# Optimization experiments

Measured on AMD Instinct MI355X. Metric: run time of the kernel, lower is better.

Reference implementation:

```python
import jax, jax.numpy as jnp
import numpy as np

B, N_LR, N_HR, D, NH, L, K = 16, 256, 512, 512, 8, 4, 4
FF = 4 * D

def _ln(x, g, b):
    m = jnp.mean(x, -1, keepdims=True)
    v = jnp.var(x, -1, keepdims=True)
    return (x - m) * jax.lax.rsqrt(v + 1e-5) * g + b

def _gelu(x):
    return jax.nn.gelu(x, approximate=False)  # torch nn.GELU default = exact

def _attn(x, qkvW, qkvb, projW, projb, bias):
    b, n, d = x.shape
    hd = d // NH
    qkv = (x @ qkvW + qkvb).reshape(b, n, 3, NH, hd).transpose(2, 0, 3, 1, 4)
    q, k, v = qkv[0], qkv[1], qkv[2]
    a = jnp.einsum('bhnd,bhmd->bhnm', q, k) * (hd ** -0.5)
    if bias is not None:
        a = a + bias
    a = jax.nn.softmax(a, axis=-1)
    o = jnp.einsum('bhnm,bhmd->bhnd', a, v).transpose(0, 2, 1, 3).reshape(b, n, d)
    return o @ projW + projb

def _ffn(x, W1, b1, W2, b2):
    return _gelu(x @ W1 + b1) @ W2 + b2

def setup_inputs() -> dict:
    key = jax.random.key(0)
    ks = iter(jax.random.split(key, 64))
    def rn(shape, s=0.02):
        return jax.random.normal(next(ks), shape, jnp.float32) * s
    inp = {}
    A = rn((B, N_LR, N_LR), 1.0)
    A = 0.5 * (A + A.transpose(0, 2, 1))  # symmetric weighted adjacency
    inp['A_lr'] = A
    inp['X_lr'] = A  # node features = adjacency rows, as in the original model
    inp['ip_W'] = rn((N_LR, D)); inp['ip_b'] = jnp.zeros(D)
    inp['ip_g'] = jnp.ones(D); inp['ip_bt'] = jnp.zeros(D)
    inp['e_n1g'] = jnp.ones((L, D)); inp['e_n1b'] = jnp.zeros((L, D))
    inp['e_qkvW'] = rn((L, D, 3 * D)); inp['e_qkvb'] = jnp.zeros((L, 3 * D))
    inp['e_projW'] = rn((L, D, D)); inp['e_projb'] = jnp.zeros((L, D))
    inp['e_ebW'] = rn((L, NH), 1.0); inp['e_ebs'] = jnp.full((L,), 0.1)
    inp['e_n2g'] = jnp.ones((L, D)); inp['e_n2b'] = jnp.zeros((L, D))
    inp['e_f1W'] = rn((L, D, FF)); inp['e_f1b'] = jnp.zeros((L, FF))
    inp['e_f2W'] = rn((L, FF, D)); inp['e_f2b'] = jnp.zeros((L, D))
    inp['encn_g'] = jnp.ones(D); inp['encn_b'] = jnp.zeros(D)
    inp['up1W'] = rn((N_LR, N_HR)); inp['up1b'] = jnp.zeros(N_HR)
    inp['up2W'] = rn((N_HR, N_HR)); inp['up2b'] = jnp.zeros(N_HR)
    inp['r_n1g'] = jnp.ones(D); inp['r_n1b'] = jnp.zeros(D)
    inp['r_qkvW'] = rn((D, 3 * D)); inp['r_qkvb'] = jnp.zeros(3 * D)
    inp['r_projW'] = rn((D, D)); inp['r_projb'] = jnp.zeros(D)
    inp['r_n2g'] = jnp.ones(D); inp['r_n2b'] = jnp.zeros(D)
    inp['r_f1W'] = rn((D, FF)); inp['r_f1b'] = jnp.zeros(FF)
    inp['r_f2W'] = rn((FF, D)); inp['r_f2b'] = jnp.zeros(D)
    inp['hrn_g'] = jnp.ones(D); inp['hrn_b'] = jnp.zeros(D)
    inp['dec_W'] = rn((K, D, D)); inp['dec_b'] = jnp.full((1,), 3.0)
    return inp

def reference(A_lr, X_lr, ip_W, ip_b, ip_g, ip_bt, e_n1g, e_n1b, e_qkvW, e_qkvb, e_projW, e_projb, e_ebW, e_ebs, e_n2g, e_n2b, e_f1W, e_f1b, e_f2W, e_f2b, encn_g, encn_b, up1W, up1b, up2W, up2b, r_n1g, r_n1b, r_qkvW, r_qkvb, r_projW, r_projb, r_n2g, r_n2b, r_f1W, r_f1b, r_f2W, r_f2b, hrn_g, hrn_b, dec_W, dec_b):
    # input_proj: Linear -> LayerNorm -> GELU (dropout is identity in eval)
    H = _gelu(_ln(X_lr @ ip_W + ip_b, ip_g, ip_bt))  # (B, n_lr, D)
    # encoder: pre-norm blocks with additive per-head edge bias in softmax
    for l in range(L):
        bias = e_ebs[l] * A_lr[:, None, :, :] * e_ebW[l][None, :, None, None]  # (B,NH,N,N)
        H = H + _attn(_ln(H, e_n1g[l], e_n1b[l]), e_qkvW[l], e_qkvb[l], e_projW[l], e_projb[l], bias)
        H = H + _ffn(_ln(H, e_n2g[l], e_n2b[l]), e_f1W[l], e_f1b[l], e_f2W[l], e_f2b[l])
    H = _ln(H, encn_g, encn_b)
    # upsample n_lr -> n_hr along node axis (applied on transposed H)
    Ht = H.transpose(0, 2, 1)                      # (B, D, n_lr)
    Ht = _gelu(Ht @ up1W + up1b) @ up2W + up2b     # (B, D, n_hr)
    H = Ht.transpose(0, 2, 1)                      # (B, n_hr, D)
    # HR refinement: standard pre-norm self-attention block
    H = H + _attn(_ln(H, r_n1g, r_n1b), r_qkvW, r_qkvb, r_projW, r_projb, None)
    H = H + _ffn(_ln(H, r_n2g, r_n2b), r_f1W, r_f1b, r_f2W, r_f2b)
    H = _ln(H, hrn_g, hrn_b)
    # bilinear multi-head decoder: mean_k H W_k H^T, symmetrized
    A_pred = jnp.einsum('bnd,kde,bme->bnm', H, dec_W, H) / K
    A_pred = 0.5 * (A_pred + A_pred.transpose(0, 2, 1))
    iu, ju = np.triu_indices(N_HR, k=1)
    pred = A_pred[:, iu, ju]                        # (B, n_hr*(n_hr-1)/2)
    return jax.nn.softplus(pred + dec_b[0])
```

## Files before the change

### kernel.cpp

```cpp
#include <hip/hip_runtime.h>
#include <hip/hip_bf16.h>
#include <math.h>

#define DEV __device__ __forceinline__

typedef __attribute__((ext_vector_type(8))) short bf16x8;
typedef __attribute__((ext_vector_type(4))) float f32x4;

DEV float gelu_f(float x) { return 0.5f * x * (1.0f + erff(x * 0.70710678118654752f)); }

DEV float block_reduce(float v, bool is_sum, float* red) {
#pragma unroll
  for (int off = 32; off > 0; off >>= 1) {
    float o = __shfl_down(v, off, 64);
    v = is_sum ? (v + o) : fmaxf(v, o);
  }
  __syncthreads();
  if ((threadIdx.x & 63) == 0) red[threadIdx.x >> 6] = v;
  __syncthreads();
  return is_sum ? (red[0] + red[1] + red[2] + red[3])
                : fmaxf(fmaxf(red[0], red[1]), fmaxf(red[2], red[3]));
}

DEV short bf16s(float x) {
  __hip_bfloat16 v = __float2bfloat16(x);
  return *reinterpret_cast<short*>(&v);
}

DEV void async16(void* lds, const void* g) {
  __builtin_amdgcn_global_load_lds(
      (const __attribute__((address_space(1))) unsigned int*)g,
      (__attribute__((address_space(3))) unsigned int*)lds, 16, 0, 0);
}

__global__ __launch_bounds__(256) void conv_kernel(
    const float* __restrict__ X, __hip_bfloat16* __restrict__ Y, int n) {
  int i = blockIdx.x * 256 + threadIdx.x;
  if (i < n) Y[i] = __float2bfloat16(X[i]);
}

__global__ __launch_bounds__(256) void tconv_kernel(
    const float* __restrict__ X, __hip_bfloat16* __restrict__ Y, int R, int C) {
  __shared__ float t[32][33];
  const float* xb = X + (size_t)blockIdx.z * R * C;
  __hip_bfloat16* yb = Y + (size_t)blockIdx.z * R * C;
  int c0 = blockIdx.x * 32, r0 = blockIdx.y * 32;
  int tx = threadIdx.x & 31, ty = threadIdx.x >> 5;
  for (int i = ty; i < 32; i += 8) t[i][tx] = xb[(size_t)(r0 + i) * C + c0 + tx];
  __syncthreads();
  for (int i = ty; i < 32; i += 8)
    yb[(size_t)(c0 + i) * R + r0 + tx] = __float2bfloat16(t[tx][i]);
}

__global__ __launch_bounds__(256) void build_s_kernel(
    const float* __restrict__ W, __hip_bfloat16* __restrict__ S, int D, int Kk) {
  int i = blockIdx.x * 256 + threadIdx.x;
  if (i >= D * D) return;
  int d = i / D, e = i % D;
  float s = 0.f;
  for (int k = 0; k < Kk; ++k) {
    s += W[(size_t)k * D * D + i];
    s += W[(size_t)k * D * D + (size_t)e * D + d];
  }
  S[i] = __float2bfloat16(s / (2.0f * Kk));
}

__global__ __launch_bounds__(256) void mgemm_kernel(
    const __hip_bfloat16* __restrict__ A, const __hip_bfloat16* __restrict__ Bt,
    const float* __restrict__ bias, const float* __restrict__ resid,
    float* __restrict__ outf, __hip_bfloat16* __restrict__ outb,
    int M, int N, int K, int act, int mgrp) {
  __shared__ __align__(16) short As[64 * 64];
  __shared__ __align__(16) short Bs[64 * 64];
  const int tid = threadIdx.x;
  const int lane = tid & 63, wave = tid >> 6;
  const int quad = lane >> 4, l15 = lane & 15;
  const int bid = blockIdx.x;
  const int g = bid & 7, sidx = bid >> 3;
  const int mt = g * mgrp + sidx % mgrp;
  const int nt = sidx / mgrp;
  const int row0 = mt * 64, col0 = nt * 64;
  const short* Ag = (const short*)A;
  const short* Bg = (const short*)Bt;
  f32x4 acc[4] = {};

  for (int k0 = 0; k0 < K; k0 += 64) {
    __syncthreads();
#pragma unroll
    for (int i = 0; i < 2; ++i) {
      int c = (wave * 2 + i) * 64 + lane;
      int r = c >> 3, pp = c & 7;
      int kc = pp ^ (r & 7);
      async16(&As[(wave * 2 + i) * 512], &Ag[(size_t)(row0 + r) * K + k0 + kc * 8]);
      async16(&Bs[(wave * 2 + i) * 512], &Bg[(size_t)(col0 + r) * K + k0 + kc * 8]);
    }
    __syncthreads();
#pragma unroll
    for (int kh = 0; kh < 2; ++kh) {
      const int ch = ((quad + kh * 4) ^ (l15 & 7)) * 8;
      bf16x8 af = *(const bf16x8*)&As[(wave * 16 + l15) * 64 + ch];
#pragma unroll
      for (int ni = 0; ni < 4; ++ni) {
        bf16x8 bq = *(const bf16x8*)&Bs[(ni * 16 + l15) * 64 + ch];
        acc[ni] = __builtin_amdgcn_mfma_f32_16x16x32_bf16(af, bq, acc[ni], 0, 0, 0);
      }
    }
  }

#pragma unroll
  for (int ni = 0; ni < 4; ++ni) {
    int cc = col0 + ni * 16 + l15;
    float bb = bias ? bias[cc] : 0.f;
#pragma unroll
    for (int r = 0; r < 4; ++r) {
      int rr = row0 + wave * 16 + quad * 4 + r;
      size_t idx = (size_t)rr * N + cc;
      float v = acc[ni][r] + bb;
      if (act) v = gelu_f(v);
      if (resid) v += resid[idx];
      if (outf) outf[idx] = v;
      if (outb) outb[idx] = __float2bfloat16(v);
    }
  }
}

__global__ __launch_bounds__(256) void qkv_gemm_kernel(
    const __hip_bfloat16* __restrict__ A, const __hip_bfloat16* __restrict__ Bt,
    const float* __restrict__ bias, __hip_bfloat16* __restrict__ qkv,
    int M, int K, int nseq, int lgn, int mgrp) {
  __shared__ __align__(16) short As[64 * 64];
  __shared__ __align__(16) short Bs[64 * 64];
  const int tid = threadIdx.x;
  const int lane = tid & 63, wave = tid >> 6;
  const int quad = lane >> 4, l15 = lane & 15;
  const int bid = blockIdx.x;
  const int g = bid & 7, sidx = bid >> 3;
  const int mt = g * mgrp + sidx % mgrp;
  const int nt = sidx / mgrp;
  const int row0 = mt * 64, col0 = nt * 64;
  const short* Ag = (const short*)A;
  const short* Bg = (const short*)Bt;
  f32x4 acc[4] = {};

  for (int k0 = 0; k0 < K; k0 += 64) {
    __syncthreads();
#pragma unroll
    for (int i = 0; i < 2; ++i) {
      int c = (wave * 2 + i) * 64 + lane;
      int r = c >> 3, pp = c & 7;
      int kc = pp ^ (r & 7);
      async16(&As[(wave * 2 + i) * 512], &Ag[(size_t)(row0 + r) * K + k0 + kc * 8]);
      async16(&Bs[(wave * 2 + i) * 512], &Bg[(size_t)(col0 + r) * K + k0 + kc * 8]);
    }
    __syncthreads();
#pragma unroll
    for (int kh = 0; kh < 2; ++kh) {
      const int ch = ((quad + kh * 4) ^ (l15 & 7)) * 8;
      bf16x8 af = *(const bf16x8*)&As[(wave * 16 + l15) * 64 + ch];
#pragma unroll
      for (int ni = 0; ni < 4; ++ni) {
        bf16x8 bq = *(const bf16x8*)&Bs[(ni * 16 + l15) * 64 + ch];
        acc[ni] = __builtin_amdgcn_mfma_f32_16x16x32_bf16(af, bq, acc[ni], 0, 0, 0);
      }
    }
  }

  const size_t PART = (size_t)M * 512;
#pragma unroll
  for (int ni = 0; ni < 4; ++ni) {
    int cc = col0 + ni * 16 + l15;
    float bb = bias ? bias[cc] : 0.f;
    int which = cc >> 9;
    int h = (cc >> 6) & 7;
    int d = cc & 63;
#pragma unroll
    for (int r = 0; r < 4; ++r) {
      int rr = row0 + wave * 16 + quad * 4 + r;
      int b = rr >> lgn;
      int nn = rr & (nseq - 1);
      float v = acc[ni][r] + bb;
      size_t dst;
      if (which == 2) {
        dst = 2 * PART + (((size_t)b * 8 + h) * 64 + d) * nseq + nn;
      } else {
        dst = (size_t)which * PART + (((size_t)b * 8 + h) * nseq + nn) * 64 + d;
      }
      qkv[dst] = __float2bfloat16(v);
    }
  }
}

__global__ __launch_bounds__(256) void fattn_kernel(
    const __hip_bfloat16* __restrict__ Qh, const __hip_bfloat16* __restrict__ Kh,
    const __hip_bfloat16* __restrict__ Vt, __hip_bfloat16* __restrict__ O,
    const __hip_bfloat16* __restrict__ Abias, const float* __restrict__ ebW,
    const float* __restrict__ ebs, int N, int lgq) {
  __shared__ __align__(16) short Ks[64][72];
  __shared__ __align__(16) short Vs[64][72];
  __shared__ __align__(16) short Ps[4][16][72];
  const int bid = blockIdx.x;
  const int g = bid & 7, s = bid >> 3;
  const int bloc = s >> (lgq + 3);
  const int rem = s & ((8 << lgq) - 1);
  const int h = rem >> lgq;
  const int qt = rem & ((1 << lgq) - 1);
  const int b = g * 2 + bloc;
  const int tid = threadIdx.x, lane = tid & 63, wave = tid >> 6;
  const int quad = lane >> 4, l15 = lane & 15;
  const size_t hb = (size_t)b * 8 + h;
  const short* Qg = (const short*)Qh + hb * N * 64;
  const short* Kg = (const short*)Kh + hb * N * 64;
  const short* Vg = (const short*)Vt + hb * 64 * N;
  const float scale = 0.125f;
  const bool hasb = (Abias != nullptr);
  const float bscale = hasb ? ebs[0] * ebW[h] : 0.f;
  const int qrow_w = qt * 64 + wave * 16;

  bf16x8 qf0 = *(const bf16x8*)&Qg[(size_t)(qrow_w + l15) * 64 + quad * 8];
  bf16x8 qf1 = *(const bf16x8*)&Qg[(size_t)(qrow_w + l15) * 64 + quad * 8 + 32];

  float m_i[4], l_i[4];
  f32x4 oacc[4] = {};
#pragma unroll
  for (int r = 0; r < 4; ++r) { m_i[r] = -1e30f; l_i[r] = 0.f; }

  for (int k0 = 0; k0 < N; k0 += 64) {
    __syncthreads();
#pragma unroll
    for (int i = 0; i < 2; ++i) {
      int idx = i * 256 + tid;
      int r = idx >> 3, ch = idx & 7;
      *(uint4*)&Ks[r][ch * 8] = *(const uint4*)&Kg[(size_t)(k0 + r) * 64 + ch * 8];
      *(uint4*)&Vs[r][ch * 8] = *(const uint4*)&Vg[(size_t)r * N + k0 + ch * 8];
    }
    __syncthreads();

    f32x4 sv[4] = {};
#pragma unroll
    for (int ni = 0; ni < 4; ++ni) {
      bf16x8 kf0 = *(const bf16x8*)&Ks[ni * 16 + l15][quad * 8];
      bf16x8 kf1 = *(const bf16x8*)&Ks[ni * 16 + l15][quad * 8 + 32];
      sv[ni] = __builtin_amdgcn_mfma_f32_16x16x32_bf16(qf0, kf0, sv[ni], 0, 0, 0);
      sv[ni] = __builtin_amdgcn_mfma_f32_16x16x32_bf16(qf1, kf1, sv[ni], 0, 0, 0);
    }
    if (hasb) {
#pragma unroll
      for (int ni = 0; ni < 4; ++ni)
#pragma unroll
        for (int r = 0; r < 4; ++r) {
          int qq = qrow_w + quad * 4 + r;
          int kk = k0 + ni * 16 + l15;
          float ab = __bfloat162float(Abias[((size_t)b * N + qq) * N + kk]);
          sv[ni][r] = sv[ni][r] * scale + bscale * ab;
        }
    } else {
#pragma unroll
      for (int ni = 0; ni < 4; ++ni)
#pragma unroll
        for (int r = 0; r < 4; ++r) sv[ni][r] *= scale;
    }

    float mt[4];
#pragma unroll
    for (int r = 0; r < 4; ++r)
      mt[r] = fmaxf(fmaxf(sv[0][r], sv[1][r]), fmaxf(sv[2][r], sv[3][r]));
#pragma unroll
    for (int off = 1; off < 16; off <<= 1)
#pragma unroll
      for (int r = 0; r < 4; ++r) mt[r] = fmaxf(mt[r], __shfl_xor(mt[r], off, 64));

    float alpha[4];
#pragma unroll
    for (int r = 0; r < 4; ++r) {
      float mn = fmaxf(m_i[r], mt[r]);
      alpha[r] = __expf(m_i[r] - mn);
      m_i[r] = mn;
    }
    float ls[4] = {0.f, 0.f, 0.f, 0.f};
#pragma unroll
    for (int ni = 0; ni < 4; ++ni)
#pragma unroll
      for (int r = 0; r < 4; ++r) {
        float p = __expf(sv[ni][r] - m_i[r]);
        sv[ni][r] = p;
        ls[r] += p;
      }
#pragma unroll
    for (int off = 1; off < 16; off <<= 1)
#pragma unroll
      for (int r = 0; r < 4; ++r) ls[r] += __shfl_xor(ls[r], off, 64);
#pragma unroll
    for (int r = 0; r < 4; ++r) l_i[r] = l_i[r] * alpha[r] + ls[r];
#pragma unroll
    for (int ni = 0; ni < 4; ++ni)
#pragma unroll
      for (int r = 0; r < 4; ++r) oacc[ni][r] *= alpha[r];

#pragma unroll
    for (int ni = 0; ni < 4; ++ni)
#pragma unroll
      for (int r = 0; r < 4; ++r)
        Ps[wave][quad * 4 + r][ni * 16 + l15] = bf16s(sv[ni][r]);

    bf16x8 pf0 = *(const bf16x8*)&Ps[wave][l15][quad * 8];
    bf16x8 pf1 = *(const bf16x8*)&Ps[wave][l15][quad * 8 + 32];
#pragma unroll
    for (int ni = 0; ni < 4; ++ni) {
      bf16x8 vf0 = *(const bf16x8*)&Vs[ni * 16 + l15][quad * 8];
      bf16x8 vf1 = *(const bf16x8*)&Vs[ni * 16 + l15][quad * 8 + 32];
      oacc[ni] = __builtin_amdgcn_mfma_f32_16x16x32_bf16(pf0, vf0, oacc[ni], 0, 0, 0);
      oacc[ni] = __builtin_amdgcn_mfma_f32_16x16x32_bf16(pf1, vf1, oacc[ni], 0, 0, 0);
    }
  }

  float inv[4];
#pragma unroll
  for (int r = 0; r < 4; ++r) inv[r] = 1.f / l_i[r];
#pragma unroll
  for (int ni = 0; ni < 4; ++ni)
#pragma unroll
    for (int r = 0; r < 4; ++r) {
      int nn = qrow_w + quad * 4 + r;
      int col = h * 64 + ni * 16 + l15;
      O[((size_t)b * N + nn) * 512 + col] = __float2bfloat16(oacc[ni][r] * inv[r]);
    }
}

__global__ __launch_bounds__(256) void dec_mfma_kernel(
    const __hip_bfloat16* __restrict__ Tb_, const __hip_bfloat16* __restrict__ Hb_,
    const float* __restrict__ dec_b, float* __restrict__ out) {
  const int Nn = 512, K = 512;
  __shared__ __align__(16) short As[64 * 64];
  __shared__ __align__(16) short Bs[64 * 64];
  int p = blockIdx.x;
  int bb = blockIdx.y;
  int it = 0, rem = p;
  while (rem >= 8 - it) { rem -= 8 - it; ++it; }
  int jt = it + rem;
  const int row0 = it * 64, col0 = jt * 64;
  const int tid = threadIdx.x;
  const int lane = tid & 63, wave = tid >> 6;
  const int quad = lane >> 4, l15 = lane & 15;
  const int wr = (wave >> 1) * 32, wc = (wave & 1) * 32;
  const short* Ag = (const short*)(Tb_ + (size_t)bb * Nn * K);
  const short* Bg = (const short*)(Hb_ + (size_t)bb * Nn * K);
  f32x4 acc[2][2] = {};

  for (int k0 = 0; k0 < K; k0 += 64) {
    __syncthreads();
#pragma unroll
    for (int i = 0; i < 2; ++i) {
      int c = (wave * 2 + i) * 64 + lane;
      int r = c >> 3, pp = c & 7;
      int kc = pp ^ (r & 7);
      async16(&As[(wave * 2 + i) * 512], &Ag[(size_t)(row0 + r) * K + k0 + kc * 8]);
      async16(&Bs[(wave * 2 + i) * 512], &Bg[(size_t)(col0 + r) * K + k0 + kc * 8]);
    }
    __syncthreads();
#pragma unroll
    for (int kh = 0; kh < 2; ++kh) {
      const int ch = ((quad + kh * 4) ^ (l15 & 7)) * 8;
      bf16x8 af[2], bq[2];
#pragma unroll
      for (int mi = 0; mi < 2; ++mi)
        af[mi] = *(const bf16x8*)&As[(wr + mi * 16 + l15) * 64 + ch];
#pragma unroll
      for (int ni = 0; ni < 2; ++ni)
        bq[ni] = *(const bf16x8*)&Bs[(wc + ni * 16 + l15) * 64 + ch];
#pragma unroll
      for (int mi = 0; mi < 2; ++mi)
#pragma unroll
        for (int ni = 0; ni < 2; ++ni)
          acc[mi][ni] = __builtin_amdgcn_mfma_f32_16x16x32_bf16(af[mi], bq[ni], acc[mi][ni], 0, 0, 0);
    }
  }

  float db = dec_b[0];
  size_t obase = (size_t)bb * ((size_t)Nn * (Nn - 1) / 2);
#pragma unroll
  for (int mi = 0; mi < 2; ++mi) {
#pragma unroll
    for (int ni = 0; ni < 2; ++ni) {
      int j = col0 + wc + ni * 16 + l15;
#pragma unroll
      for (int r = 0; r < 4; ++r) {
        int i = row0 + wr + mi * 16 + quad * 4 + r;
        if (j > i) {
          float x = acc[mi][ni][r] + db;
          float sp = fmaxf(x, 0.f) + __logf(1.f + __expf(-fabsf(x)));
          out[obase + (size_t)i * (2 * Nn - i - 1) / 2 + (j - i - 1)] = sp;
        }
      }
    }
  }
}

__global__ __launch_bounds__(256) void ln_kernel(
    const float* __restrict__ X, float* __restrict__ outf,
    __hip_bfloat16* __restrict__ outb, const float* __restrict__ g,
    const float* __restrict__ b, int D, int do_gelu) {
  __shared__ float red[4];
  int row = blockIdx.x;
  const float* x = X + (size_t)row * D;
  float s = 0.f, s2 = 0.f;
  for (int d = threadIdx.x; d < D; d += 256) {
    float v = x[d];
    s += v;
    s2 += v * v;
  }
  s = block_reduce(s, true, red);
  s2 = block_reduce(s2, true, red);
  float mean = s / D;
  float var = s2 / D - mean * mean;
  float inv = rsqrtf(var + 1e-5f);
  for (int d = threadIdx.x; d < D; d += 256) {
    float v = (x[d] - mean) * inv * g[d] + b[d];
    if (do_gelu) v = gelu_f(v);
    if (outf) outf[(size_t)row * D + d] = v;
    if (outb) outb[(size_t)row * D + d] = __float2bfloat16(v);
  }
}

template <typename T>
__global__ __launch_bounds__(256) void transpose_kernel(
    const T* __restrict__ X, T* __restrict__ Y, int R, int C) {
  __shared__ T t[32][33];
  const T* xb = X + (size_t)blockIdx.z * R * C;
  T* yb = Y + (size_t)blockIdx.z * R * C;
  int c0 = blockIdx.x * 32, r0 = blockIdx.y * 32;
  int tx = threadIdx.x & 31, ty = threadIdx.x >> 5;
  for (int i = ty; i < 32; i += 8) t[i][tx] = xb[(size_t)(r0 + i) * C + c0 + tx];
  __syncthreads();
  for (int i = ty; i < 32; i += 8) yb[(size_t)(c0 + i) * R + r0 + tx] = t[tx][i];
}

extern "C" void kernel_launch(void* const* d_in, const int* in_sizes, int n_in,
                              void* d_out, int out_size, void* d_ws, size_t ws_size,
                              hipStream_t stream) {
  const float *A_lr = (const float*)d_in[0], *X_lr = (const float*)d_in[1],
              *ip_W = (const float*)d_in[2], *ip_b = (const float*)d_in[3],
              *ip_g = (const float*)d_in[4], *ip_bt = (const float*)d_in[5],
              *e_n1g = (const float*)d_in[6], *e_n1b = (const float*)d_in[7],
              *e_qkvW = (const float*)d_in[8], *e_qkvb = (const float*)d_in[9],
              *e_projW = (const float*)d_in[10], *e_projb = (const float*)d_in[11],
              *e_ebW = (const float*)d_in[12], *e_ebs = (const float*)d_in[13],
              *e_n2g = (const float*)d_in[14], *e_n2b = (const float*)d_in[15],
              *e_f1W = (const float*)d_in[16], *e_f1b = (const float*)d_in[17],
              *e_f2W = (const float*)d_in[18], *e_f2b = (const float*)d_in[19],
              *encn_g = (const float*)d_in[20], *encn_b = (const float*)d_in[21],
              *up1W = (const float*)d_in[22], *up1b = (const float*)d_in[23],
              *up2W = (const float*)d_in[24], *up2b = (const float*)d_in[25],
              *r_n1g = (const float*)d_in[26], *r_n1b = (const float*)d_in[27],
              *r_qkvW = (const float*)d_in[28], *r_qkvb = (const float*)d_in[29],
              *r_projW = (const float*)d_in[30], *r_projb = (const float*)d_in[31],
              *r_n2g = (const float*)d_in[32], *r_n2b = (const float*)d_in[33],
              *r_f1W = (const float*)d_in[34], *r_f1b = (const float*)d_in[35],
              *r_f2W = (const float*)d_in[36], *r_f2b = (const float*)d_in[37],
              *hrn_g = (const float*)d_in[38], *hrn_b = (const float*)d_in[39],
              *dec_W = (const float*)d_in[40], *dec_b = (const float*)d_in[41];

  const int Bb = 16, NLR = 256, NHR = 512, Dm = 512, NHh = 8, FF = 2048, Ll = 4;
  typedef __hip_bfloat16 bf;

  float* ws = (float*)d_ws;
  float* H = ws;
  float* Hf = ws + 4194304;
  bf* XNb = (bf*)(ws + 8388608);
  bf* AOb = (bf*)(ws + 10485760);
  bf* BIGb = (bf*)(ws + 12582912);
  bf* WB = (bf*)(ws + 20971520);
  bf* Xlrb = (bf*)(ws + 29229056);

  size_t o = 0;
  bf* ipWt = WB + o;   o += (size_t)512 * 256;
  bf* eqkvT = WB + o;  o += (size_t)4 * 1536 * 512;
  bf* eprojT = WB + o; o += (size_t)4 * 512 * 512;
  bf* ef1T = WB + o;   o += (size_t)4 * 2048 * 512;
  bf* ef2T = WB + o;   o += (size_t)4 * 512 * 2048;
  bf* up1T = WB + o;   o += (size_t)512 * 256;
  bf* up2T = WB + o;   o += (size_t)512 * 512;
  bf* rqkvT = WB + o;  o += (size_t)1536 * 512;
  bf* rprojT = WB + o; o += (size_t)512 * 512;
  bf* rf1T = WB + o;   o += (size_t)2048 * 512;
  bf* rf2T = WB + o;   o += (size_t)512 * 2048;
  bf* Sb = WB + o;     o += (size_t)512 * 512;

  bf* Q_e = BIGb;
  bf* K_e = BIGb + 2097152;
  bf* V_e = BIGb + 4194304;
  bf* Q_r = BIGb;
  bf* K_r = BIGb + 4194304;
  bf* V_r = BIGb + 8388608;
  bf* Albrb = Xlrb;

  tconv_kernel<<<dim3(16, 8, 1), 256, 0, stream>>>(ip_W, ipWt, 256, 512);
  tconv_kernel<<<dim3(48, 16, 4), 256, 0, stream>>>(e_qkvW, eqkvT, 512, 1536);
  tconv_kernel<<<dim3(16, 16, 4), 256, 0, stream>>>(e_projW, eprojT, 512, 512);
  tconv_kernel<<<dim3(64, 16, 4), 256, 0, stream>>>(e_f1W, ef1T, 512, 2048);
  tconv_kernel<<<dim3(16, 64, 4), 256, 0, stream>>>(e_f2W, ef2T, 2048, 512);
  tconv_kernel<<<dim3(16, 8, 1), 256, 0, stream>>>(up1W, up1T, 256, 512);
  tconv_kernel<<<dim3(16, 16, 1), 256, 0, stream>>>(up2W, up2T, 512, 512);
  tconv_kernel<<<dim3(48, 16, 1), 256, 0, stream>>>(r_qkvW, rqkvT, 512, 1536);
  tconv_kernel<<<dim3(16, 16, 1), 256, 0, stream>>>(r_projW, rprojT, 512, 512);
  tconv_kernel<<<dim3(64, 16, 1), 256, 0, stream>>>(r_f1W, rf1T, 512, 2048);
  tconv_kernel<<<dim3(16, 64, 1), 256, 0, stream>>>(r_f2W, rf2T, 2048, 512);
  conv_kernel<<<(1048576 + 255) / 256, 256, 0, stream>>>(X_lr, Xlrb, 1048576);
  build_s_kernel<<<(512 * 512 + 255) / 256, 256, 0, stream>>>(dec_W, Sb, Dm, 4);

  mgemm_kernel<<<64 * 8, 256, 0, stream>>>(
      Xlrb, ipWt, ip_b, nullptr, Hf, nullptr, Bb * NLR, Dm, NLR, 0, 8);
  ln_kernel<<<Bb * NLR, 256, 0, stream>>>(Hf, H, nullptr, ip_g, ip_bt, Dm, 1);
  conv_kernel<<<(1048576 + 255) / 256, 256, 0, stream>>>(A_lr, Albrb, 1048576);

  for (int l = 0; l < Ll; ++l) {
    ln_kernel<<<Bb * NLR, 256, 0, stream>>>(H, nullptr, XNb, e_n1g + l * Dm, e_n1b + l * Dm, Dm, 0);
    qkv_gemm_kernel<<<64 * 24, 256, 0, stream>>>(
        XNb, eqkvT + (size_t)l * 1536 * 512, e_qkvb + l * 1536, BIGb,
        Bb * NLR, Dm, NLR, 8, 8);
    fattn_kernel<<<16 * 8 * 4, 256, 0, stream>>>(
        Q_e, K_e, V_e, AOb, Albrb, e_ebW + l * NHh, e_ebs + l, NLR, 2);
    mgemm_kernel<<<64 * 8, 256, 0, stream>>>(
        AOb, eprojT + (size_t)l * 512 * 512, e_projb + l * Dm, H,
        H, nullptr, Bb * NLR, Dm, Dm, 0, 8);
    ln_kernel<<<Bb * NLR, 256, 0, stream>>>(H, nullptr, XNb, e_n2g + l * Dm, e_n2b + l * Dm, Dm, 0);
    mgemm_kernel<<<64 * 32, 256, 0, stream>>>(
        XNb, ef1T + (size_t)l * 2048 * 512, e_f1b + l * FF, nullptr,
        nullptr, BIGb, Bb * NLR, FF, Dm, 1, 8);
    mgemm_kernel<<<64 * 8, 256, 0, stream>>>(
        BIGb, ef2T + (size_t)l * 512 * 2048, e_f2b + l * Dm, H,
        H, nullptr, Bb * NLR, Dm, FF, 0, 8);
  }

  ln_kernel<<<Bb * NLR, 256, 0, stream>>>(H, nullptr, XNb, encn_g, encn_b, Dm, 0);
  transpose_kernel<bf><<<dim3(16, 8, Bb), 256, 0, stream>>>(XNb, AOb, NLR, Dm);
  mgemm_kernel<<<128 * 8, 256, 0, stream>>>(
      AOb, up1T, up1b, nullptr, nullptr, BIGb, Bb * Dm, NHR, NLR, 1, 16);
  mgemm_kernel<<<128 * 8, 256, 0, stream>>>(
      BIGb, up2T, up2b, nullptr, Hf, nullptr, Bb * Dm, NHR, NHR, 0, 16);
  transpose_kernel<float><<<dim3(16, 16, Bb), 256, 0, stream>>>(Hf, H, Dm, NHR);

  ln_kernel<<<Bb * NHR, 256, 0, stream>>>(H, nullptr, XNb, r_n1g, r_n1b, Dm, 0);
  qkv_gemm_kernel<<<128 * 24, 256, 0, stream>>>(
      XNb, rqkvT, r_qkvb, BIGb, Bb * NHR, Dm, NHR, 9, 16);
  fattn_kernel<<<16 * 8 * 8, 256, 0, stream>>>(
      Q_r, K_r, V_r, AOb, nullptr, nullptr, nullptr, NHR, 3);
  mgemm_kernel<<<128 * 8, 256, 0, stream>>>(
      AOb, rprojT, r_projb, H, H, nullptr, Bb * NHR, Dm, Dm, 0, 16);
  ln_kernel<<<Bb * NHR, 256, 0, stream>>>(H, nullptr, XNb, r_n2g, r_n2b, Dm, 0);
  mgemm_kernel<<<128 * 32, 256, 0, stream>>>(
      XNb, rf1T, r_f1b, nullptr, nullptr, BIGb, Bb * NHR, FF, Dm, 1, 16);
  mgemm_kernel<<<128 * 8, 256, 0, stream>>>(
      BIGb, rf2T, r_f2b, H, H, nullptr, Bb * NHR, Dm, FF, 0, 16);

  ln_kernel<<<Bb * NHR, 256, 0, stream>>>(H, nullptr, XNb, hrn_g, hrn_b, Dm, 0);
  mgemm_kernel<<<128 * 8, 256, 0, stream>>>(
      XNb, Sb, nullptr, nullptr, nullptr, AOb, Bb * NHR, Dm, Dm, 0, 16);
  dec_mfma_kernel<<<dim3(36, Bb), 256, 0, stream>>>(
      AOb, XNb, dec_b, (float*)d_out);
}
```

Before: 911.1 us.

## Double-buffer GEMM and attention LDS tiles, batch weight conversions into one launch

```diff
diff --git a/kernel.cpp b/kernel.cpp
--- a/kernel.cpp
+++ b/kernel.cpp
@@ -33,18 +33,40 @@
       (__attribute__((address_space(3))) unsigned int*)lds, 16, 0, 0);
 }
 
-__global__ __launch_bounds__(256) void conv_kernel(
-    const float* __restrict__ X, __hip_bfloat16* __restrict__ Y, int n) {
+__global__ __launch_bounds__(256) void conv2_kernel(
+    const float* __restrict__ X1, __hip_bfloat16* __restrict__ Y1,
+    const float* __restrict__ X2, __hip_bfloat16* __restrict__ Y2, int n) {
   int i = blockIdx.x * 256 + threadIdx.x;
-  if (i < n) Y[i] = __float2bfloat16(X[i]);
-}
-
-__global__ __launch_bounds__(256) void tconv_kernel(
-    const float* __restrict__ X, __hip_bfloat16* __restrict__ Y, int R, int C) {
+  if (i < n) {
+    Y1[i] = __float2bfloat16(X1[i]);
+    Y2[i] = __float2bfloat16(X2[i]);
+  }
+}
+
+struct CvArgs {
+  const float* s[11];
+  __hip_bfloat16* d[11];
+};
+
+__global__ __launch_bounds__(256) void multi_tconv_kernel(CvArgs a) {
+  const int Rj[11] = {256, 512, 512, 512, 2048, 256, 512, 512, 512, 512, 2048};
+  const int Cj[11] = {512, 1536, 512, 2048, 512, 512, 512, 1536, 512, 2048, 512};
+  const int Nj[11] = {1, 4, 4, 4, 4, 1, 1, 1, 1, 1, 1};
   __shared__ float t[32][33];
-  const float* xb = X + (size_t)blockIdx.z * R * C;
-  __hip_bfloat16* yb = Y + (size_t)blockIdx.z * R * C;
-  int c0 = blockIdx.x * 32, r0 = blockIdx.y * 32;
+  int rem = blockIdx.x, j = 0;
+  for (; j < 11; ++j) {
+    int tj = (Rj[j] >> 5) * (Cj[j] >> 5) * Nj[j];
+    if (rem < tj) break;
+    rem -= tj;
+  }
+  const int R = Rj[j], C = Cj[j];
+  const int perb = (R >> 5) * (C >> 5);
+  const int z = rem / perb;
+  const int tt = rem % perb;
+  const int tc = C >> 5;
+  const int r0 = (tt / tc) << 5, c0 = (tt % tc) << 5;
+  const float* xb = a.s[j] + (size_t)z * R * C;
+  __hip_bfloat16* yb = a.d[j] + (size_t)z * R * C;
   int tx = threadIdx.x & 31, ty = threadIdx.x >> 5;
   for (int i = ty; i < 32; i += 8) t[i][tx] = xb[(size_t)(r0 + i) * C + c0 + tx];
   __syncthreads();
@@ -70,8 +92,8 @@
     const float* __restrict__ bias, const float* __restrict__ resid,
     float* __restrict__ outf, __hip_bfloat16* __restrict__ outb,
     int M, int N, int K, int act, int mgrp) {
-  __shared__ __align__(16) short As[64 * 64];
-  __shared__ __align__(16) short Bs[64 * 64];
+  __shared__ __align__(16) short As[2][64 * 64];
+  __shared__ __align__(16) short Bs[2][64 * 64];
   const int tid = threadIdx.x;
   const int lane = tid & 63, wave = tid >> 6;
   const int quad = lane >> 4, l15 = lane & 15;
@@ -82,26 +104,32 @@
   const int row0 = mt * 64, col0 = nt * 64;
   const short* Ag = (const short*)A;
   const short* Bg = (const short*)Bt;
-  f32x4 acc[4] = {};
-
-  for (int k0 = 0; k0 < K; k0 += 64) {
-    __syncthreads();
+
+  auto stage = [&](int bsel, int k0) {
 #pragma unroll
     for (int i = 0; i < 2; ++i) {
       int c = (wave * 2 + i) * 64 + lane;
       int r = c >> 3, pp = c & 7;
       int kc = pp ^ (r & 7);
-      async16(&As[(wave * 2 + i) * 512], &Ag[(size_t)(row0 + r) * K + k0 + kc * 8]);
-      async16(&Bs[(wave * 2 + i) * 512], &Bg[(size_t)(col0 + r) * K + k0 + kc * 8]);
-    }
+      async16(&As[bsel][(wave * 2 + i) * 512], &Ag[(size_t)(row0 + r) * K + k0 + kc * 8]);
+      async16(&Bs[bsel][(wave * 2 + i) * 512], &Bg[(size_t)(col0 + r) * K + k0 + kc * 8]);
+    }
+  };
+
+  f32x4 acc[4] = {};
+  const int nk = K >> 6;
+  stage(0, 0);
+  for (int t = 0; t < nk; ++t) {
+    const int cur = t & 1;
     __syncthreads();
+    if (t + 1 < nk) stage(cur ^ 1, (t + 1) << 6);
 #pragma unroll
     for (int kh = 0; kh < 2; ++kh) {
       const int ch = ((quad + kh * 4) ^ (l15 & 7)) * 8;
-      bf16x8 af = *(const bf16x8*)&As[(wave * 16 + l15) * 64 + ch];
+      bf16x8 af = *(const bf16x8*)&As[cur][(wave * 16 + l15) * 64 + ch];
 #pragma unroll
       for (int ni = 0; ni < 4; ++ni) {
-        bf16x8 bq = *(const bf16x8*)&Bs[(ni * 16 + l15) * 64 + ch];
+        bf16x8 bq = *(const bf16x8*)&Bs[cur][(ni * 16 + l15) * 64 + ch];
         acc[ni] = __builtin_amdgcn_mfma_f32_16x16x32_bf16(af, bq, acc[ni], 0, 0, 0);
       }
     }
@@ -128,8 +156,8 @@
     const __hip_bfloat16* __restrict__ A, const __hip_bfloat16* __restrict__ Bt,
     const float* __restrict__ bias, __hip_bfloat16* __restrict__ qkv,
     int M, int K, int nseq, int lgn, int mgrp) {
-  __shared__ __align__(16) short As[64 * 64];
-  __shared__ __align__(16) short Bs[64 * 64];
+  __shared__ __align__(16) short As[2][64 * 64];
+  __shared__ __align__(16) short Bs[2][64 * 64];
   const int tid = threadIdx.x;
   const int lane = tid & 63, wave = tid >> 6;
   const int quad = lane >> 4, l15 = lane & 15;
@@ -140,26 +168,32 @@
   const int row0 = mt * 64, col0 = nt * 64;
   const short* Ag = (const short*)A;
   const short* Bg = (const short*)Bt;
-  f32x4 acc[4] = {};
-
-  for (int k0 = 0; k0 < K; k0 += 64) {
-    __syncthreads();
+
+  auto stage = [&](int bsel, int k0) {
 #pragma unroll
     for (int i = 0; i < 2; ++i) {
       int c = (wave * 2 + i) * 64 + lane;
       int r = c >> 3, pp = c & 7;
       int kc = pp ^ (r & 7);
-      async16(&As[(wave * 2 + i) * 512], &Ag[(size_t)(row0 + r) * K + k0 + kc * 8]);
-      async16(&Bs[(wave * 2 + i) * 512], &Bg[(size_t)(col0 + r) * K + k0 + kc * 8]);
-    }
+      async16(&As[bsel][(wave * 2 + i) * 512], &Ag[(size_t)(row0 + r) * K + k0 + kc * 8]);
+      async16(&Bs[bsel][(wave * 2 + i) * 512], &Bg[(size_t)(col0 + r) * K + k0 + kc * 8]);
+    }
+  };
+
+  f32x4 acc[4] = {};
+  const int nk = K >> 6;
+  stage(0, 0);
+  for (int t = 0; t < nk; ++t) {
+    const int cur = t & 1;
     __syncthreads();
+    if (t + 1 < nk) stage(cur ^ 1, (t + 1) << 6);
 #pragma unroll
     for (int kh = 0; kh < 2; ++kh) {
       const int ch = ((quad + kh * 4) ^ (l15 & 7)) * 8;
-      bf16x8 af = *(const bf16x8*)&As[(wave * 16 + l15) * 64 + ch];
+      bf16x8 af = *(const bf16x8*)&As[cur][(wave * 16 + l15) * 64 + ch];
 #pragma unroll
       for (int ni = 0; ni < 4; ++ni) {
-        bf16x8 bq = *(const bf16x8*)&Bs[(ni * 16 + l15) * 64 + ch];
+        bf16x8 bq = *(const bf16x8*)&Bs[cur][(ni * 16 + l15) * 64 + ch];
         acc[ni] = __builtin_amdgcn_mfma_f32_16x16x32_bf16(af, bq, acc[ni], 0, 0, 0);
       }
     }
@@ -195,8 +229,8 @@
     const __hip_bfloat16* __restrict__ Vt, __hip_bfloat16* __restrict__ O,
     const __hip_bfloat16* __restrict__ Abias, const float* __restrict__ ebW,
     const float* __restrict__ ebs, int N, int lgq) {
-  __shared__ __align__(16) short Ks[64][72];
-  __shared__ __align__(16) short Vs[64][72];
+  __shared__ __align__(16) short Ks[2][64 * 64];
+  __shared__ __align__(16) short Vs[2][64 * 64];
   __shared__ __align__(16) short Ps[4][16][72];
   const int bid = blockIdx.x;
   const int g = bid & 7, s = bid >> 3;
@@ -216,32 +250,43 @@
   const float bscale = hasb ? ebs[0] * ebW[h] : 0.f;
   const int qrow_w = qt * 64 + wave * 16;
 
-  bf16x8 qf0 = *(const bf16x8*)&Qg[(size_t)(qrow_w + l15) * 64 + quad * 8];
-  bf16x8 qf1 = *(const bf16x8*)&Qg[(size_t)(qrow_w + l15) * 64 + quad * 8 + 32];
+  auto stageKV = [&](int bsel, int k0) {
+#pragma unroll
+    for (int i = 0; i < 2; ++i) {
+      int c = (wave * 2 + i) * 64 + lane;
+      int r = c >> 3, pp = c & 7;
+      int kc = pp ^ (r & 7);
+      async16(&Ks[bsel][(wave * 2 + i) * 512], &Kg[(size_t)(k0 + r) * 64 + kc * 8]);
+      async16(&Vs[bsel][(wave * 2 + i) * 512], &Vg[(size_t)r * N + k0 + kc * 8]);
+    }
+  };
+
+  bf16x8 qf[2];
+  qf[0] = *(const bf16x8*)&Qg[(size_t)(qrow_w + l15) * 64 + quad * 8];
+  qf[1] = *(const bf16x8*)&Qg[(size_t)(qrow_w + l15) * 64 + quad * 8 + 32];
 
   float m_i[4], l_i[4];
   f32x4 oacc[4] = {};
 #pragma unroll
   for (int r = 0; r < 4; ++r) { m_i[r] = -1e30f; l_i[r] = 0.f; }
 
-  for (int k0 = 0; k0 < N; k0 += 64) {
+  const int ntl = N >> 6;
+  stageKV(0, 0);
+  for (int t = 0; t < ntl; ++t) {
+    const int cur = t & 1;
+    const int k0 = t << 6;
     __syncthreads();
-#pragma unroll
-    for (int i = 0; i < 2; ++i) {
-      int idx = i * 256 + tid;
-      int r = idx >> 3, ch = idx & 7;
-      *(uint4*)&Ks[r][ch * 8] = *(const uint4*)&Kg[(size_t)(k0 + r) * 64 + ch * 8];
-      *(uint4*)&Vs[r][ch * 8] = *(const uint4*)&Vg[(size_t)r * N + k0 + ch * 8];
-    }
-    __syncthreads();
+    if (t + 1 < ntl) stageKV(cur ^ 1, (t + 1) << 6);
 
     f32x4 sv[4] = {};
 #pragma unroll
-    for (int ni = 0; ni < 4; ++ni) {
-      bf16x8 kf0 = *(const bf16x8*)&Ks[ni * 16 + l15][quad * 8];
-      bf16x8 kf1 = *(const bf16x8*)&Ks[ni * 16 + l15][quad * 8 + 32];
-      sv[ni] = __builtin_amdgcn_mfma_f32_16x16x32_bf16(qf0, kf0, sv[ni], 0, 0, 0);
-      sv[ni] = __builtin_amdgcn_mfma_f32_16x16x32_bf16(qf1, kf1, sv[ni], 0, 0, 0);
+    for (int kh = 0; kh < 2; ++kh) {
+      const int ch = ((quad + kh * 4) ^ (l15 & 7)) * 8;
+#pragma unroll
+      for (int ni = 0; ni < 4; ++ni) {
+        bf16x8 kf = *(const bf16x8*)&Ks[cur][(ni * 16 + l15) * 64 + ch];
+        sv[ni] = __builtin_amdgcn_mfma_f32_16x16x32_bf16(qf[kh], kf, sv[ni], 0, 0, 0);
+      }
     }
     if (hasb) {
 #pragma unroll
@@ -305,11 +350,13 @@
     bf16x8 pf0 = *(const bf16x8*)&Ps[wave][l15][quad * 8];
     bf16x8 pf1 = *(const bf16x8*)&Ps[wave][l15][quad * 8 + 32];
 #pragma unroll
-    for (int ni = 0; ni < 4; ++ni) {
-      bf16x8 vf0 = *(const bf16x8*)&Vs[ni * 16 + l15][quad * 8];
-      bf16x8 vf1 = *(const bf16x8*)&Vs[ni * 16 + l15][quad * 8 + 32];
-      oacc[ni] = __builtin_amdgcn_mfma_f32_16x16x32_bf16(pf0, vf0, oacc[ni], 0, 0, 0);
-      oacc[ni] = __builtin_amdgcn_mfma_f32_16x16x32_bf16(pf1, vf1, oacc[ni], 0, 0, 0);
+    for (int kh = 0; kh < 2; ++kh) {
+      const int ch = ((quad + kh * 4) ^ (l15 & 7)) * 8;
+#pragma unroll
+      for (int ni = 0; ni < 4; ++ni) {
+        bf16x8 vf = *(const bf16x8*)&Vs[cur][(ni * 16 + l15) * 64 + ch];
+        oacc[ni] = __builtin_amdgcn_mfma_f32_16x16x32_bf16(kh ? pf1 : pf0, vf, oacc[ni], 0, 0, 0);
+      }
     }
   }
 
@@ -330,8 +377,8 @@
     const __hip_bfloat16* __restrict__ Tb_, const __hip_bfloat16* __restrict__ Hb_,
     const float* __restrict__ dec_b, float* __restrict__ out) {
   const int Nn = 512, K = 512;
-  __shared__ __align__(16) short As[64 * 64];
-  __shared__ __align__(16) short Bs[64 * 64];
+  __shared__ __align__(16) short As[2][64 * 64];
+  __shared__ __align__(16) short Bs[2][64 * 64];
   int p = blockIdx.x;
   int bb = blockIdx.y;
   int it = 0, rem = p;
@@ -344,29 +391,35 @@
   const int wr = (wave >> 1) * 32, wc = (wave & 1) * 32;
   const short* Ag = (const short*)(Tb_ + (size_t)bb * Nn * K);
   const short* Bg = (const short*)(Hb_ + (size_t)bb * Nn * K);
-  f32x4 acc[2][2] = {};
-
-  for (int k0 = 0; k0 < K; k0 += 64) {
-    __syncthreads();
+
+  auto stage = [&](int bsel, int k0) {
 #pragma unroll
     for (int i = 0; i < 2; ++i) {
       int c = (wave * 2 + i) * 64 + lane;
       int r = c >> 3, pp = c & 7;
       int kc = pp ^ (r & 7);
-      async16(&As[(wave * 2 + i) * 512], &Ag[(size_t)(row0 + r) * K + k0 + kc * 8]);
-      async16(&Bs[(wave * 2 + i) * 512], &Bg[(size_t)(col0 + r) * K + k0 + kc * 8]);
-    }
+      async16(&As[bsel][(wave * 2 + i) * 512], &Ag[(size_t)(row0 + r) * K + k0 + kc * 8]);
+      async16(&Bs[bsel][(wave * 2 + i) * 512], &Bg[(size_t)(col0 + r) * K + k0 + kc * 8]);
+    }
+  };
+
+  f32x4 acc[2][2] = {};
+  const int nk = K >> 6;
+  stage(0, 0);
+  for (int t = 0; t < nk; ++t) {
+    const int cur = t & 1;
     __syncthreads();
+    if (t + 1 < nk) stage(cur ^ 1, (t + 1) << 6);
 #pragma unroll
     for (int kh = 0; kh < 2; ++kh) {
       const int ch = ((quad + kh * 4) ^ (l15 & 7)) * 8;
       bf16x8 af[2], bq[2];
 #pragma unroll
       for (int mi = 0; mi < 2; ++mi)
-        af[mi] = *(const bf16x8*)&As[(wr + mi * 16 + l15) * 64 + ch];
+        af[mi] = *(const bf16x8*)&As[cur][(wr + mi * 16 + l15) * 64 + ch];
 #pragma unroll
       for (int ni = 0; ni < 2; ++ni)
-        bq[ni] = *(const bf16x8*)&Bs[(wc + ni * 16 + l15) * 64 + ch];
+        bq[ni] = *(const bf16x8*)&Bs[cur][(wc + ni * 16 + l15) * 64 + ch];
 #pragma unroll
       for (int mi = 0; mi < 2; ++mi)
 #pragma unroll
@@ -470,6 +523,7 @@
   bf* BIGb = (bf*)(ws + 12582912);
   bf* WB = (bf*)(ws + 20971520);
   bf* Xlrb = (bf*)(ws + 29229056);
+  bf* Albrb = (bf*)(ws + 29753344);
 
   size_t o = 0;
   bf* ipWt = WB + o;   o += (size_t)512 * 256;
@@ -491,26 +545,27 @@
   bf* Q_r = BIGb;
   bf* K_r = BIGb + 4194304;
   bf* V_r = BIGb + 8388608;
-  bf* Albrb = Xlrb;
-
-  tconv_kernel<<<dim3(16, 8, 1), 256, 0, stream>>>(ip_W, ipWt, 256, 512);
-  tconv_kernel<<<dim3(48, 16, 4), 256, 0, stream>>>(e_qkvW, eqkvT, 512, 1536);
-  tconv_kernel<<<dim3(16, 16, 4), 256, 0, stream>>>(e_projW, eprojT, 512, 512);
-  tconv_kernel<<<dim3(64, 16, 4), 256, 0, stream>>>(e_f1W, ef1T, 512, 2048);
-  tconv_kernel<<<dim3(16, 64, 4), 256, 0, stream>>>(e_f2W, ef2T, 2048, 512);
-  tconv_kernel<<<dim3(16, 8, 1), 256, 0, stream>>>(up1W, up1T, 256, 512);
-  tconv_kernel<<<dim3(16, 16, 1), 256, 0, stream>>>(up2W, up2T, 512, 512);
-  tconv_kernel<<<dim3(48, 16, 1), 256, 0, stream>>>(r_qkvW, rqkvT, 512, 1536);
-  tconv_kernel<<<dim3(16, 16, 1), 256, 0, stream>>>(r_projW, rprojT, 512, 512);
-  tconv_kernel<<<dim3(64, 16, 1), 256, 0, stream>>>(r_f1W, rf1T, 512, 2048);
-  tconv_kernel<<<dim3(16, 64, 1), 256, 0, stream>>>(r_f2W, rf2T, 2048, 512);
-  conv_kernel<<<(1048576 + 255) / 256, 256, 0, stream>>>(X_lr, Xlrb, 1048576);
+
+  CvArgs cv;
+  cv.s[0] = ip_W;   cv.d[0] = ipWt;
+  cv.s[1] = e_qkvW; cv.d[1] = eqkvT;
+  cv.s[2] = e_projW; cv.d[2] = eprojT;
+  cv.s[3] = e_f1W;  cv.d[3] = ef1T;
+  cv.s[4] = e_f2W;  cv.d[4] = ef2T;
+  cv.s[5] = up1W;   cv.d[5] = up1T;
+  cv.s[6] = up2W;   cv.d[6] = up2T;
+  cv.s[7] = r_qkvW; cv.d[7] = rqkvT;
+  cv.s[8] = r_projW; cv.d[8] = rprojT;
+  cv.s[9] = r_f1W;  cv.d[9] = rf1T;
+  cv.s[10] = r_f2W; cv.d[10] = rf2T;
+  multi_tconv_kernel<<<15872, 256, 0, stream>>>(cv);
+  conv2_kernel<<<(1048576 + 255) / 256, 256, 0, stream>>>(
+      X_lr, Xlrb, A_lr, Albrb, 1048576);
   build_s_kernel<<<(512 * 512 + 255) / 256, 256, 0, stream>>>(dec_W, Sb, Dm, 4);
 
   mgemm_kernel<<<64 * 8, 256, 0, stream>>>(
       Xlrb, ipWt, ip_b, nullptr, Hf, nullptr, Bb * NLR, Dm, NLR, 0, 8);
   ln_kernel<<<Bb * NLR, 256, 0, stream>>>(Hf, H, nullptr, ip_g, ip_bt, Dm, 1);
-  conv_kernel<<<(1048576 + 255) / 256, 256, 0, stream>>>(A_lr, Albrb, 1048576);
 
   for (int l = 0; l < Ll; ++l) {
     ln_kernel<<<Bb * NLR, 256, 0, stream>>>(H, nullptr, XNb, e_n1g + l * Dm, e_n1b + l * Dm, Dm, 0);
```

New measurement: 901.4 us. No clear change (-1.1%).
